# Kernel optimization log

Hardware: AMD Instinct MI355X
Metric: run time of the kernel (lower is better)

Reference implementation:

```python
import jax, jax.numpy as jnp
import numpy as np

CHANNEL = 16
SCALE_D = 0.05


def _bilinear_plane(coords, img_chw, scale_0, scale_1):
    # coords: [N, 2]; img_chw: [C, H, W]
    img = jnp.transpose(img_chw, (1, 2, 0))  # [H, W, C]
    D0, D1 = img.shape[0], img.shape[1]
    x = (coords[:, 0] / scale_0 + 1.0) * (D0 - 1) * 0.5
    y = (coords[:, 1] / scale_1 + 1.0) * (D1 - 1) * 0.5
    x0 = jnp.floor(x)
    x1 = x0 + 1.0
    y0 = jnp.floor(y)
    y1 = y0 + 1.0
    # weights use the UNCLAMPED floor values (matches torch code)
    wa = (x1 - x) * (y1 - y)
    wb = (x - x0) * (y1 - y)
    wc = (x1 - x) * (y - y0)
    wd = (x - x0) * (y - y0)
    x0i = jnp.clip(x0, 0, D0 - 2).astype(jnp.int32)
    x1i = jnp.clip(x1, 1, D0 - 1).astype(jnp.int32)
    y0i = jnp.clip(y0, 0, D1 - 2).astype(jnp.int32)
    y1i = jnp.clip(y1, 1, D1 - 1).astype(jnp.int32)
    Ia = img[x0i, y0i]  # [N, C]
    Ib = img[x1i, y0i]
    Ic = img[x0i, y1i]
    Id = img[x1i, y1i]
    return (wa[:, None] * Ia + wb[:, None] * Ib
            + wc[:, None] * Ic + wd[:, None] * Id)


def setup_inputs() -> dict:
    key = jax.random.key(0)
    k1, k2 = jax.random.split(key)
    N = 4_000_000
    res = 512
    xyz = jax.random.uniform(k1, (N, 3), dtype=jnp.float32, minval=-1.0, maxval=1.0)
    # z coordinate lives in the thin slab [-scale_d, scale_d]
    xyz = xyz.at[:, 2].multiply(SCALE_D)
    feature_maps = jax.random.normal(k2, (3 * CHANNEL, res, res), dtype=jnp.float32)
    return {"xyz": xyz, "feature_maps": feature_maps}


def reference(xyz, feature_maps):
    hh, ww = feature_maps.shape[-2], feature_maps.shape[-1]
    planes = feature_maps.reshape(3, CHANNEL, hh, ww)
    xy = xyz[:, jnp.array([0, 1])]
    yz = xyz[:, jnp.array([1, 2])]
    zx = xyz[:, jnp.array([2, 0])]
    f_xy = _bilinear_plane(xy, planes[0], 1.0, 1.0)
    f_yz = _bilinear_plane(yz, planes[2], 1.0, SCALE_D)
    f_zx = _bilinear_plane(zx, planes[1], SCALE_D, 1.0)
    return jnp.concatenate([f_xy, f_yz, f_zx], axis=-1)  # [N, 3*C]
```

## Files before the change

kernel.cpp:

```cpp
#include <hip/hip_runtime.h>
#include <hip/hip_fp16.h>

#define RES 512
#define CHAN 16
#define HW (RES * RES)
#define PLANE_F (CHAN * HW)

__global__ __launch_bounds__(256) void triplane_transpose_f16(
    const float* __restrict__ src, uint4* __restrict__ dst) {
  int b    = blockIdx.x;
  int p    = b >> 11;
  int rem  = b & 2047;
  int h    = rem >> 2;
  int strip= rem & 3;
  int half = threadIdx.x & 1;
  int w    = (strip << 7) + (threadIdx.x >> 1);

  const float* s = src + (size_t)(p * CHAN + half * 8) * HW + h * RES + w;

  uint u[4];
#pragma unroll
  for (int k = 0; k < 4; ++k) {
    float f0 = s[(size_t)(2 * k + 0) * HW];
    float f1 = s[(size_t)(2 * k + 1) * HW];
    uint lo = (uint)__half_as_ushort(__float2half_rn(f0));
    uint hi = (uint)__half_as_ushort(__float2half_rn(f1));
    u[k] = lo | (hi << 16);
  }
  dst[((size_t)p * HW + h * RES + w) * 2 + half] = make_uint4(u[0], u[1], u[2], u[3]);
}

__device__ __forceinline__ float4 h4_to_f4(uint2 u) {
  __half2 h0 = *reinterpret_cast<const __half2*>(&u.x);
  __half2 h1 = *reinterpret_cast<const __half2*>(&u.y);
  float2 f0 = __half22float2(h0);
  float2 f1 = __half22float2(h1);
  return make_float4(f0.x, f0.y, f1.x, f1.y);
}

template <bool TRANSPOSED>
__global__ __launch_bounds__(256) void triplane_gather(
    const float* __restrict__ xyz, const void* __restrict__ fm,
    float* __restrict__ out, int n12) {
  int gid = blockIdx.x * 256 + threadIdx.x;
  if (gid >= n12) return;

  int p  = gid / 12;
  int q  = gid - p * 12;
  int s  = q >> 2;
  int cq = q & 3;

  float x = xyz[p * 3 + 0];
  float y = xyz[p * 3 + 1];
  float z = xyz[p * 3 + 2];
  float zs = z / 0.05f;

  float a  = (s == 0) ? x : ((s == 1) ? y : zs);
  float b  = (s == 0) ? y : ((s == 1) ? zs : x);
  int   pl = (s == 0) ? 0 : ((s == 1) ? 2 : 1);

  float u = (a + 1.0f) * 255.5f;
  float v = (b + 1.0f) * 255.5f;

  float x0 = floorf(u), y0 = floorf(v);
  float x1 = x0 + 1.0f, y1 = y0 + 1.0f;

  float wa = (x1 - u) * (y1 - v);
  float wb = (u - x0) * (y1 - v);
  float wc = (x1 - u) * (v - y0);
  float wd = (u - x0) * (v - y0);

  int x0i = (int)fminf(fmaxf(x0, 0.0f), 510.0f);
  int x1i = (int)fminf(fmaxf(x1, 1.0f), 511.0f);
  int y0i = (int)fminf(fmaxf(y0, 0.0f), 510.0f);
  int y1i = (int)fminf(fmaxf(y1, 1.0f), 511.0f);

  float4 r;
  if (TRANSPOSED) {
    const uint2* base = (const uint2*)fm + (size_t)pl * (HW * 4);
    uint2 A = base[(size_t)(x0i * RES + y0i) * 4 + cq];
    uint2 B = base[(size_t)(x1i * RES + y0i) * 4 + cq];
    uint2 C = base[(size_t)(x0i * RES + y1i) * 4 + cq];
    uint2 D = base[(size_t)(x1i * RES + y1i) * 4 + cq];
    float4 fA = h4_to_f4(A);
    float4 fB = h4_to_f4(B);
    float4 fC = h4_to_f4(C);
    float4 fD = h4_to_f4(D);
    r.x = wa * fA.x + wb * fB.x + wc * fC.x + wd * fD.x;
    r.y = wa * fA.y + wb * fB.y + wc * fC.y + wd * fD.y;
    r.z = wa * fA.z + wb * fB.z + wc * fC.z + wd * fD.z;
    r.w = wa * fA.w + wb * fB.w + wc * fC.w + wd * fD.w;
  } else {
    const float* fbase = (const float*)fm + (size_t)pl * PLANE_F + (size_t)(cq * 4) * HW;
    float acc[4];
#pragma unroll
    for (int j = 0; j < 4; ++j) {
      const float* ch = fbase + (size_t)j * HW;
      float A = ch[x0i * RES + y0i];
      float B = ch[x1i * RES + y0i];
      float C = ch[x0i * RES + y1i];
      float D = ch[x1i * RES + y1i];
      acc[j] = wa * A + wb * B + wc * C + wd * D;
    }
    r = make_float4(acc[0], acc[1], acc[2], acc[3]);
  }

  ((float4*)out)[gid] = r;
}

extern "C" void kernel_launch(void* const* d_in, const int* in_sizes, int n_in,
                              void* d_out, int out_size, void* d_ws, size_t ws_size,
                              hipStream_t stream) {
  const float* xyz = (const float*)d_in[0];
  const float* fm  = (const float*)d_in[1];
  float* out = (float*)d_out;

  int N   = in_sizes[0] / 3;
  int n12 = N * 12;
  int grid = (n12 + 255) / 256;

  size_t need = (size_t)3 * HW * CHAN * sizeof(unsigned short);
  if (ws_size >= need) {
    triplane_transpose_f16<<<3 * 2048, 256, 0, stream>>>(fm, (uint4*)d_ws);
    triplane_gather<true><<<grid, 256, 0, stream>>>(xyz, d_ws, out, n12);
  } else {
    triplane_gather<false><<<grid, 256, 0, stream>>>(xyz, fm, out, n12);
  }
}
```

Measured before the change: 1.240 ms.

## Bin points into Morton-ordered 3D cells before gathering for cache locality

Adds a counting sort of query points into a 32^3 grid of cells keyed by Morton code, using a histogram, a single-block scan and an atomic scatter into a packed float4 buffer that carries the original index. The gather kernel then walks the sorted points, so neighbouring threads sample nearby texels and L2/MALL reuse on the fp16 planes improves. Output is written back to each point's original index. It also remaps block IDs so that each XCD handles a contiguous range of sorted work. The cost is several extra kernel launches, atomics and extra traffic for cellid and the sorted buffer, and output writes become scattered.

```diff
diff --git a/kernel.cpp b/kernel.cpp
--- a/kernel.cpp
+++ b/kernel.cpp
@@ -5,6 +5,8 @@
 #define CHAN 16
 #define HW (RES * RES)
 #define PLANE_F (CHAN * HW)
+#define CG 32
+#define NCELLS (CG * CG * CG)
 
 __global__ __launch_bounds__(256) void triplane_transpose_f16(
     const float* __restrict__ src, uint4* __restrict__ dst) {
@@ -30,6 +32,75 @@
   dst[((size_t)p * HW + h * RES + w) * 2 + half] = make_uint4(u[0], u[1], u[2], u[3]);
 }
 
+__device__ __forceinline__ unsigned part1by2(unsigned x) {
+  x &= 0x3ff;
+  x = (x | (x << 16)) & 0x030000FF;
+  x = (x | (x << 8))  & 0x0300F00F;
+  x = (x | (x << 4))  & 0x030C30C3;
+  x = (x | (x << 2))  & 0x09249249;
+  return x;
+}
+
+__device__ __forceinline__ int cell_coord(float v) {
+  int c = (int)((v + 1.0f) * (0.5f * CG));
+  return min(max(c, 0), CG - 1);
+}
+
+__global__ __launch_bounds__(256) void cell_hist(
+    const float* __restrict__ xyz, int N,
+    unsigned* __restrict__ cellid, unsigned* __restrict__ hist) {
+  int p = blockIdx.x * 256 + threadIdx.x;
+  if (p >= N) return;
+  float x = xyz[3 * p + 0];
+  float y = xyz[3 * p + 1];
+  float z = xyz[3 * p + 2];
+  int cx = cell_coord(x);
+  int cy = cell_coord(y);
+  int cz = cell_coord(z * 20.0f);
+  unsigned key = part1by2((unsigned)cx) | (part1by2((unsigned)cy) << 1) |
+                 (part1by2((unsigned)cz) << 2);
+  cellid[p] = key;
+  atomicAdd(&hist[key], 1u);
+}
+
+__global__ __launch_bounds__(256) void zero_u32(unsigned* __restrict__ a, int n) {
+  int i = blockIdx.x * 256 + threadIdx.x;
+  if (i < n) a[i] = 0u;
+}
+
+__global__ __launch_bounds__(1024) void scan_cells(
+    const unsigned* __restrict__ hist, unsigned* __restrict__ cursor) {
+  __shared__ unsigned s[1024];
+  int tid = threadIdx.x;
+  unsigned local[32];
+  unsigned sum = 0;
+  int base = tid * 32;
+#pragma unroll
+  for (int i = 0; i < 32; ++i) { local[i] = hist[base + i]; sum += local[i]; }
+  s[tid] = sum;
+  __syncthreads();
+  for (int d = 1; d < 1024; d <<= 1) {
+    unsigned v = (tid >= d) ? s[tid - d] : 0u;
+    __syncthreads();
+    s[tid] += v;
+    __syncthreads();
+  }
+  unsigned run = s[tid] - sum;
+#pragma unroll
+  for (int i = 0; i < 32; ++i) { cursor[base + i] = run; run += local[i]; }
+}
+
+__global__ __launch_bounds__(256) void cell_scatter(
+    const float* __restrict__ xyz, const unsigned* __restrict__ cellid,
+    unsigned* __restrict__ cursor, float4* __restrict__ sorted, int N) {
+  int p = blockIdx.x * 256 + threadIdx.x;
+  if (p >= N) return;
+  unsigned key = cellid[p];
+  unsigned pos = atomicAdd(&cursor[key], 1u);
+  sorted[pos] = make_float4(xyz[3 * p + 0], xyz[3 * p + 1], xyz[3 * p + 2],
+                            __int_as_float(p));
+}
+
 __device__ __forceinline__ float4 h4_to_f4(uint2 u) {
   __half2 h0 = *reinterpret_cast<const __half2*>(&u.x);
   __half2 h1 = *reinterpret_cast<const __half2*>(&u.y);
@@ -38,6 +109,66 @@
   return make_float4(f0.x, f0.y, f1.x, f1.y);
 }
 
+__device__ __forceinline__ float4 bilerp_f16(
+    const void* fm, int pl, int cq, float a, float b) {
+  float u = (a + 1.0f) * 255.5f;
+  float v = (b + 1.0f) * 255.5f;
+  float x0 = floorf(u), y0 = floorf(v);
+  float x1 = x0 + 1.0f, y1 = y0 + 1.0f;
+  float wa = (x1 - u) * (y1 - v);
+  float wb = (u - x0) * (y1 - v);
+  float wc = (x1 - u) * (v - y0);
+  float wd = (u - x0) * (v - y0);
+  int x0i = (int)fminf(fmaxf(x0, 0.0f), 510.0f);
+  int x1i = (int)fminf(fmaxf(x1, 1.0f), 511.0f);
+  int y0i = (int)fminf(fmaxf(y0, 0.0f), 510.0f);
+  int y1i = (int)fminf(fmaxf(y1, 1.0f), 511.0f);
+  const uint2* base = (const uint2*)fm + (size_t)pl * (HW * 4);
+  uint2 A = base[(size_t)(x0i * RES + y0i) * 4 + cq];
+  uint2 B = base[(size_t)(x1i * RES + y0i) * 4 + cq];
+  uint2 C = base[(size_t)(x0i * RES + y1i) * 4 + cq];
+  uint2 D = base[(size_t)(x1i * RES + y1i) * 4 + cq];
+  float4 fA = h4_to_f4(A), fB = h4_to_f4(B), fC = h4_to_f4(C), fD = h4_to_f4(D);
+  float4 r;
+  r.x = wa * fA.x + wb * fB.x + wc * fC.x + wd * fD.x;
+  r.y = wa * fA.y + wb * fB.y + wc * fC.y + wd * fD.y;
+  r.z = wa * fA.z + wb * fB.z + wc * fC.z + wd * fD.z;
+  r.w = wa * fA.w + wb * fB.w + wc * fC.w + wd * fD.w;
+  return r;
+}
+
+__global__ __launch_bounds__(256) void triplane_gather_sorted(
+    const float4* __restrict__ sorted, const void* __restrict__ fm,
+    float* __restrict__ out, int n12, int nwg) {
+  int b   = blockIdx.x;
+  int q8  = nwg >> 3;
+  int r8  = nwg & 7;
+  int xcd = b & 7;
+  int i   = b >> 3;
+  int sb  = (xcd < r8 ? xcd * (q8 + 1) : r8 * (q8 + 1) + (xcd - r8) * q8) + i;
+
+  int item = sb * 256 + (int)threadIdx.x;
+  if (item >= n12) return;
+
+  int sp = item / 12;
+  int q  = item - sp * 12;
+  int s  = q >> 2;
+  int cq = q & 3;
+
+  float4 sx = sorted[sp];
+  float x  = sx.x;
+  float y  = sx.y;
+  float zs = sx.z / 0.05f;
+  int   po = __float_as_int(sx.w);
+
+  float a  = (s == 0) ? x : ((s == 1) ? y : zs);
+  float bb = (s == 0) ? y : ((s == 1) ? zs : x);
+  int   pl = (s == 0) ? 0 : ((s == 1) ? 2 : 1);
+
+  float4 r = bilerp_f16(fm, pl, cq, a, bb);
+  ((float4*)out)[(size_t)po * 12 + q] = r;
+}
+
 template <bool TRANSPOSED>
 __global__ __launch_bounds__(256) void triplane_gather(
     const float* __restrict__ xyz, const void* __restrict__ fm,
@@ -56,41 +187,25 @@
   float zs = z / 0.05f;
 
   float a  = (s == 0) ? x : ((s == 1) ? y : zs);
-  float b  = (s == 0) ? y : ((s == 1) ? zs : x);
+  float bb = (s == 0) ? y : ((s == 1) ? zs : x);
   int   pl = (s == 0) ? 0 : ((s == 1) ? 2 : 1);
-
-  float u = (a + 1.0f) * 255.5f;
-  float v = (b + 1.0f) * 255.5f;
-
-  float x0 = floorf(u), y0 = floorf(v);
-  float x1 = x0 + 1.0f, y1 = y0 + 1.0f;
-
-  float wa = (x1 - u) * (y1 - v);
-  float wb = (u - x0) * (y1 - v);
-  float wc = (x1 - u) * (v - y0);
-  float wd = (u - x0) * (v - y0);
-
-  int x0i = (int)fminf(fmaxf(x0, 0.0f), 510.0f);
-  int x1i = (int)fminf(fmaxf(x1, 1.0f), 511.0f);
-  int y0i = (int)fminf(fmaxf(y0, 0.0f), 510.0f);
-  int y1i = (int)fminf(fmaxf(y1, 1.0f), 511.0f);
 
   float4 r;
   if (TRANSPOSED) {
-    const uint2* base = (const uint2*)fm + (size_t)pl * (HW * 4);
-    uint2 A = base[(size_t)(x0i * RES + y0i) * 4 + cq];
-    uint2 B = base[(size_t)(x1i * RES + y0i) * 4 + cq];
-    uint2 C = base[(size_t)(x0i * RES + y1i) * 4 + cq];
-    uint2 D = base[(size_t)(x1i * RES + y1i) * 4 + cq];
-    float4 fA = h4_to_f4(A);
-    float4 fB = h4_to_f4(B);
-    float4 fC = h4_to_f4(C);
-    float4 fD = h4_to_f4(D);
-    r.x = wa * fA.x + wb * fB.x + wc * fC.x + wd * fD.x;
-    r.y = wa * fA.y + wb * fB.y + wc * fC.y + wd * fD.y;
-    r.z = wa * fA.z + wb * fB.z + wc * fC.z + wd * fD.z;
-    r.w = wa * fA.w + wb * fB.w + wc * fC.w + wd * fD.w;
+    r = bilerp_f16(fm, pl, cq, a, bb);
   } else {
+    float u = (a + 1.0f) * 255.5f;
+    float v = (bb + 1.0f) * 255.5f;
+    float x0 = floorf(u), y0 = floorf(v);
+    float x1 = x0 + 1.0f, y1 = y0 + 1.0f;
+    float wa = (x1 - u) * (y1 - v);
+    float wb = (u - x0) * (y1 - v);
+    float wc = (x1 - u) * (v - y0);
+    float wd = (u - x0) * (v - y0);
+    int x0i = (int)fminf(fmaxf(x0, 0.0f), 510.0f);
+    int x1i = (int)fminf(fmaxf(x1, 1.0f), 511.0f);
+    int y0i = (int)fminf(fmaxf(y0, 0.0f), 510.0f);
+    int y1i = (int)fminf(fmaxf(y1, 1.0f), 511.0f);
     const float* fbase = (const float*)fm + (size_t)pl * PLANE_F + (size_t)(cq * 4) * HW;
     float acc[4];
 #pragma unroll
@@ -104,7 +219,6 @@
     }
     r = make_float4(acc[0], acc[1], acc[2], acc[3]);
   }
-
   ((float4*)out)[gid] = r;
 }
 
@@ -119,8 +233,31 @@
   int n12 = N * 12;
   int grid = (n12 + 255) / 256;
 
-  size_t need = (size_t)3 * HW * CHAN * sizeof(unsigned short);
-  if (ws_size >= need) {
+  size_t off_planes = 0;
+  size_t sz_planes  = (size_t)3 * HW * CHAN * sizeof(unsigned short);
+  size_t off_hist   = off_planes + sz_planes;
+  size_t off_cursor = off_hist + (size_t)NCELLS * 4;
+  size_t off_cellid = off_cursor + (size_t)NCELLS * 4;
+  size_t off_sorted = off_cellid + (size_t)N * 4;
+  size_t need_full  = off_sorted + (size_t)N * 16;
+
+  char* ws = (char*)d_ws;
+
+  if (ws_size >= need_full) {
+    unsigned* hist   = (unsigned*)(ws + off_hist);
+    unsigned* cursor = (unsigned*)(ws + off_cursor);
+    unsigned* cellid = (unsigned*)(ws + off_cellid);
+    float4*   sorted = (float4*)(ws + off_sorted);
+    void*     planes = (void*)(ws + off_planes);
+
+    int gN = (N + 255) / 256;
+    triplane_transpose_f16<<<3 * 2048, 256, 0, stream>>>(fm, (uint4*)planes);
+    zero_u32<<<(2 * NCELLS + 255) / 256, 256, 0, stream>>>(hist, 2 * NCELLS);
+    cell_hist<<<gN, 256, 0, stream>>>(xyz, N, cellid, hist);
+    scan_cells<<<1, 1024, 0, stream>>>(hist, cursor);
+    cell_scatter<<<gN, 256, 0, stream>>>(xyz, cellid, cursor, sorted, N);
+    triplane_gather_sorted<<<grid, 256, 0, stream>>>(sorted, planes, out, n12, grid);
+  } else if (ws_size >= sz_planes) {
     triplane_transpose_f16<<<3 * 2048, 256, 0, stream>>>(fm, (uint4*)d_ws);
     triplane_gather<true><<<grid, 256, 0, stream>>>(xyz, d_ws, out, n12);
   } else {
```

After: 1.522 ms. 1.23x slower.
